# Kernel optimization log

Hardware: AMD Instinct MI355X
Metric: run time of the kernel (lower is better)

The kernel has to match this reference:

```python
import jax, jax.numpy as jnp
import numpy as np

N, D, T = 4096, 256, 32
GAMMA = 1.0 / 256.0  # 1/d
ALPHA = 1.0


def _rbf_kernel(X, Y, gamma):
    # K[i, j] = exp(-gamma * ||X[i] - Y[j]||^2), vectorized (replaces the
    # original per-(i,j) Python double loop).
    x2 = jnp.sum(X * X, axis=1)  # [n]
    y2 = jnp.sum(Y * Y, axis=1)  # [m]
    d2 = x2[:, None] + y2[None, :] - 2.0 * (X @ Y.T)  # [n, m]
    d2 = jnp.maximum(d2, 0.0)  # numerical guard; exact form is non-negative
    return jnp.exp(-gamma * d2)


def setup_inputs() -> dict:
    key = jax.random.key(0)
    kx, ky = jax.random.split(key)
    X = jax.random.normal(kx, (N, D), dtype=jnp.float32)
    y = jax.random.normal(ky, (N, T), dtype=jnp.float32)
    return {"X": X, "y": y}


def reference(X, y):
    # fit: K = rbf(X, X); dual = solve(K + alpha*I, y)
    K = _rbf_kernel(X, X, GAMMA)  # [N, N]
    A = K + ALPHA * jnp.eye(N, dtype=K.dtype)
    dual_coef = jnp.linalg.solve(A, y)  # [N, T]
    # predict(X): original recomputes rbf(X, X) == K, then K @ dual_coef
    y_pred = K @ dual_coef  # [N, T]
    return y_pred
```

## Files before the change

### kernel.cpp

```cpp
#include <hip/hip_runtime.h>
#include <math.h>

#define NN 4096
#define DD 256
#define TT 32
#define GAMMA (1.0f/256.0f)
#define ITERS 10
#define JBP 8
#define JCH 512
#define IB  128
#define BROW (JCH + 8)
#define KB_PAD 40

typedef __attribute__((ext_vector_type(8))) _Float16 f16x8;
typedef __attribute__((ext_vector_type(4))) _Float16 f16x4;
typedef __attribute__((ext_vector_type(4))) float f32x4;

__global__ __launch_bounds__(256) void setup(const float* __restrict__ X,
                                             float* __restrict__ x2,
                                             _Float16* __restrict__ Xh,
                                             const float* __restrict__ y,
                                             float* __restrict__ r, float* __restrict__ x,
                                             _Float16* __restrict__ vh,
                                             _Float16* __restrict__ vl,
                                             float* __restrict__ rrp) {
    const int b = blockIdx.x, tid = threadIdx.x;
    const int wid = tid >> 6, lane = tid & 63;
    if (b < 1024) {
        int row = b * 4 + wid;
        const float* xr = X + (size_t)row * DD;
        float4 v = *(const float4*)(xr + lane * 4);
        float s = v.x * v.x + v.y * v.y + v.z * v.z + v.w * v.w;
        #pragma unroll
        for (int o = 32; o; o >>= 1) s += __shfl_down(s, o);
        if (lane == 0) x2[row] = s;
        f16x4 h;
        h[0] = (_Float16)v.x; h[1] = (_Float16)v.y; h[2] = (_Float16)v.z; h[3] = (_Float16)v.w;
        *(f16x4*)(Xh + (size_t)row * DD + lane * 4) = h;
    } else {
        int bb = b - 1024;
        int t = bb >> 3, c = bb & 7;
        float s = 0.f;
        #pragma unroll
        for (int pass = 0; pass < 2; ++pass) {
            int i = c * 512 + pass * 256 + tid;
            float v = y[(size_t)i * TT + t];
            size_t off = (size_t)t * NN + i;
            r[off] = v; x[off] = 0.f;
            _Float16 h = (_Float16)v;
            vh[off] = h; vl[off] = (_Float16)(v - (float)h);
            s += v * v;
        }
        #pragma unroll
        for (int o = 32; o; o >>= 1) s += __shfl_down(s, o);
        __shared__ float red[4];
        if (lane == 0) red[wid] = s;
        __syncthreads();
        if (tid == 0) rrp[t * 8 + c] = red[0] + red[1] + red[2] + red[3];
    }
}

__global__ __launch_bounds__(256) void k_build(const _Float16* __restrict__ Xh,
                                               const float* __restrict__ x2,
                                               _Float16* __restrict__ Kh) {
    __shared__ _Float16 As[128 * KB_PAD];
    __shared__ _Float16 Bs[256 * KB_PAD];
    const int i0 = blockIdx.x * 128, j0 = blockIdx.y * 256;
    const int tid = threadIdx.x;
    const int wid = tid >> 6, lane = tid & 63;
    const int wr = wid >> 1, wc = wid & 1;
    const int l15 = lane & 15, l4 = lane >> 4;
    f32x4 acc[4][8] = {};
    for (int kc = 0; kc < DD; kc += 32) {
        __syncthreads();
        #pragma unroll
        for (int s = 0; s < 2; ++s) {
            int idx = s * 256 + tid;
            int row = idx >> 2, c = idx & 3;
            *(uint4*)(As + row * KB_PAD + c * 8) =
                *(const uint4*)(Xh + (size_t)(i0 + row) * DD + kc + c * 8);
        }
        #pragma unroll
        for (int s = 0; s < 4; ++s) {
            int idx = s * 256 + tid;
            int row = idx >> 2, c = idx & 3;
            *(uint4*)(Bs + row * KB_PAD + c * 8) =
                *(const uint4*)(Xh + (size_t)(j0 + row) * DD + kc + c * 8);
        }
        __syncthreads();
        f16x8 af[4], bfr[8];
        #pragma unroll
        for (int m = 0; m < 4; ++m)
            af[m] = *(const f16x8*)(As + (wr * 64 + m * 16 + l15) * KB_PAD + l4 * 8);
        #pragma unroll
        for (int n = 0; n < 8; ++n)
            bfr[n] = *(const f16x8*)(Bs + (wc * 128 + n * 16 + l15) * KB_PAD + l4 * 8);
        #pragma unroll
        for (int m = 0; m < 4; ++m)
            #pragma unroll
            for (int n = 0; n < 8; ++n)
                acc[m][n] = __builtin_amdgcn_mfma_f32_16x16x32_f16(af[m], bfr[n], acc[m][n], 0, 0, 0);
    }
    #pragma unroll
    for (int m = 0; m < 4; ++m) {
        #pragma unroll
        for (int rg = 0; rg < 4; ++rg) {
            int i = i0 + wr * 64 + m * 16 + l4 * 4 + rg;
            float x2i = x2[i];
            #pragma unroll
            for (int n = 0; n < 8; ++n) {
                int j = j0 + wc * 128 + n * 16 + l15;
                float d2 = fmaxf(x2i + x2[j] - 2.f * acc[m][n][rg], 0.f);
                Kh[(size_t)i * NN + j] = (_Float16)__expf(-GAMMA * d2);
            }
        }
    }
}

template<int RED>
__global__ __launch_bounds__(512) void matvec_part(const _Float16* __restrict__ Kh,
                                                   const _Float16* __restrict__ vh,
                                                   const _Float16* __restrict__ vl,
                                                   const float* __restrict__ r,
                                                   float* __restrict__ part,
                                                   float* __restrict__ rKvp) {
    __shared__ __align__(16) _Float16 Bbuf[2 * 32 * BROW];
    __shared__ float redb[8][33];
    _Float16* Bh = Bbuf;
    _Float16* Bl = Bbuf + 32 * BROW;
    const int ib = blockIdx.x;
    const int jb = blockIdx.y;
    const int bid = jb * 32 + ib;
    const int tid = threadIdx.x;
    const int wid = tid >> 6, lane = tid & 63;
    const int l15 = lane & 15, l4 = lane >> 4;
    #pragma unroll
    for (int s = 0; s < 4; ++s) {
        int c = s * 512 + tid;
        int row = c >> 6, col8 = c & 63;
        *(uint4*)(Bh + row * BROW + col8 * 8) =
            *(const uint4*)(vh + (size_t)row * NN + jb * JCH + col8 * 8);
        *(uint4*)(Bl + row * BROW + col8 * 8) =
            *(const uint4*)(vl + (size_t)row * NN + jb * JCH + col8 * 8);
    }
    __syncthreads();
    const _Float16* Ap  = Kh + (size_t)(ib * IB + wid * 16 + l15) * NN + jb * JCH + l4 * 8;
    const _Float16* bhp = Bh + l15 * BROW + l4 * 8;
    const _Float16* blp = Bl + l15 * BROW + l4 * 8;
    f32x4 acc0 = {}, acc1 = {};
    #pragma unroll 4
    for (int jc = 0; jc < JCH; jc += 32) {
        f16x8 a   = *(const f16x8*)(Ap + jc);
        f16x8 bh0 = *(const f16x8*)(bhp + jc);
        f16x8 bh1 = *(const f16x8*)(bhp + 16 * BROW + jc);
        f16x8 bl0 = *(const f16x8*)(blp + jc);
        f16x8 bl1 = *(const f16x8*)(blp + 16 * BROW + jc);
        acc0 = __builtin_amdgcn_mfma_f32_16x16x32_f16(a, bh0, acc0, 0, 0, 0);
        acc1 = __builtin_amdgcn_mfma_f32_16x16x32_f16(a, bh1, acc1, 0, 0, 0);
        acc0 = __builtin_amdgcn_mfma_f32_16x16x32_f16(a, bl0, acc0, 0, 0, 0);
        acc1 = __builtin_amdgcn_mfma_f32_16x16x32_f16(a, bl1, acc1, 0, 0, 0);
    }
    __syncthreads();
    float* tl = (float*)Bbuf;
    #pragma unroll
    for (int rg = 0; rg < 4; ++rg) {
        tl[(wid * 32 + l15) * 17 + l4 * 4 + rg]      = acc0[rg];
        tl[(wid * 32 + 16 + l15) * 17 + l4 * 4 + rg] = acc1[rg];
    }
    __syncthreads();
    #pragma unroll
    for (int q = 0; q < 8; ++q) {
        int idx = q * 64 + lane;
        int t = idx >> 4, il = idx & 15;
        int gi = ib * IB + wid * 16 + il;
        float val = tl[(wid * 32 + t) * 17 + il];
        part[((size_t)jb * TT + t) * NN + gi] = val;
        if (RED) {
            float cq = r[(size_t)t * NN + gi] * val;
            #pragma unroll
            for (int o = 8; o; o >>= 1) cq += __shfl_down(cq, o);
            if (il == 0) redb[wid][t] = cq;
        }
    }
    if (RED) {
        __syncthreads();
        if (tid < 32) {
            float s = 0.f;
            #pragma unroll
            for (int u = 0; u < 8; ++u) s += redb[u][tid];
            rKvp[tid * 256 + bid] = s;
        }
    }
}

__global__ __launch_bounds__(512) void cupd(const float* __restrict__ part, float* __restrict__ r,
                                            float* __restrict__ p, float* __restrict__ s_,
                                            float* __restrict__ x,
                                            _Float16* __restrict__ vh,
                                            _Float16* __restrict__ vl,
                                            const float* __restrict__ rrp_in,
                                            float* __restrict__ rrp_out,
                                            const float* __restrict__ rKvp,
                                            const float* __restrict__ scal_in,
                                            float* __restrict__ scal_out,
                                            int first, int last) {
    const int t = blockIdx.x, c = blockIdx.y, tid = threadIdx.x;
    const int wid = tid >> 6, lane = tid & 63;
    __shared__ float sc2[2];
    __shared__ float red[8];
    if (wid == 0) {
        float rw_ = 0.f;
        #pragma unroll
        for (int u = 0; u < 4; ++u) rw_ += rKvp[t * 256 + u * 64 + lane];
        float rr_ = (lane < 8) ? rrp_in[t * 8 + lane] : 0.f;
        #pragma unroll
        for (int o = 32; o; o >>= 1) { rw_ += __shfl_down(rw_, o); rr_ += __shfl_down(rr_, o); }
        if (lane == 0) {
            float rr = rr_;
            float rw = rw_ + rr;
            float alpha, beta;
            if (first) { beta = 0.f; alpha = rr / rw; }
            else {
                float ap = scal_in[t], rrprev = scal_in[TT + t];
                beta = rr / rrprev;
                alpha = rr / (rw - (beta / ap) * rr);
            }
            sc2[0] = alpha; sc2[1] = beta;
            if (c == 0) { scal_out[t] = alpha; scal_out[TT + t] = rr; }
        }
    }
    __syncthreads();
    const float alpha = sc2[0], beta = sc2[1];
    int i = c * 512 + tid;
    size_t off = (size_t)t * NN + i;
    float s = 0.f;
    #pragma unroll
    for (int b = 0; b < JBP; ++b) s += part[((size_t)b * TT + t) * NN + i];
    float rv = r[off];
    float wv = s + rv;
    float pn = first ? rv : fmaf(beta, p[off], rv);
    float sn = first ? wv : fmaf(beta, s_[off], wv);
    p[off] = pn; s_[off] = sn;
    float xn = x[off] + alpha * pn;
    x[off] = xn;
    float rn = rv - alpha * sn;
    r[off] = rn;
    float vout = last ? xn : rn;
    _Float16 h = (_Float16)vout;
    vh[off] = h; vl[off] = (_Float16)(vout - (float)h);
    float v = rn * rn;
    #pragma unroll
    for (int o = 32; o; o >>= 1) v += __shfl_down(v, o);
    if (lane == 0) red[wid] = v;
    __syncthreads();
    if (tid == 0) {
        float tot = 0.f;
        #pragma unroll
        for (int u = 0; u < 8; ++u) tot += red[u];
        rrp_out[t * 8 + c] = tot;
    }
}

__global__ __launch_bounds__(256) void predict_out(const float* __restrict__ part,
                                                   float* __restrict__ out) {
    __shared__ float st[TT][65];
    const int i0 = blockIdx.x * 64;
    const int tid = threadIdx.x;
    #pragma unroll
    for (int ph = 0; ph < 8; ++ph) {
        int idx = ph * 256 + tid;
        int il = idx & 63, t = idx >> 6;
        float s = 0.f;
        #pragma unroll
        for (int b = 0; b < JBP; ++b) s += part[((size_t)b * TT + t) * NN + i0 + il];
        st[t][il] = s;
    }
    __syncthreads();
    #pragma unroll
    for (int ph = 0; ph < 8; ++ph) {
        int idx = ph * 256 + tid;
        int t = idx & 31, il = idx >> 5;
        out[(size_t)(i0 + il) * TT + t] = st[t][il];
    }
}

extern "C" void kernel_launch(void* const* d_in, const int* in_sizes, int n_in,
                              void* d_out, int out_size, void* d_ws, size_t ws_size,
                              hipStream_t stream) {
    const float* X = (const float*)d_in[0];
    const float* y = (const float*)d_in[1];
    float* out = (float*)d_out;

    unsigned char* wsb = (unsigned char*)d_ws;
    _Float16* Kh = (_Float16*)wsb;  wsb += (size_t)NN * NN * 2;
    float* part  = (float*)wsb;     wsb += (size_t)JBP * TT * NN * 4;
    float* r     = (float*)wsb;     wsb += (size_t)TT * NN * 4;
    float* p     = (float*)wsb;     wsb += (size_t)TT * NN * 4;
    float* s_    = (float*)wsb;     wsb += (size_t)TT * NN * 4;
    float* x     = (float*)wsb;     wsb += (size_t)TT * NN * 4;
    _Float16* vh = (_Float16*)wsb;  wsb += (size_t)TT * NN * 2;
    _Float16* vl = (_Float16*)wsb;  wsb += (size_t)TT * NN * 2;
    _Float16* Xh = (_Float16*)wsb;  wsb += (size_t)NN * DD * 2;
    float* x2v   = (float*)wsb;     wsb += (size_t)NN * 4;
    float* rrp   = (float*)wsb;     wsb += 512 * 4;
    float* rKvp  = (float*)wsb;     wsb += (size_t)TT * 256 * 4;
    float* scal  = (float*)wsb;     wsb += 128 * 4;

    setup<<<1280, 256, 0, stream>>>(X, x2v, Xh, y, r, x, vh, vl, rrp);
    k_build<<<dim3(NN / 128, NN / 256), 256, 0, stream>>>(Xh, x2v, Kh);

    for (int j = 0; j < ITERS; ++j) {
        matvec_part<1><<<dim3(32, JBP), 512, 0, stream>>>(Kh, vh, vl, r, part, rKvp);
        cupd<<<dim3(TT, 8), 512, 0, stream>>>(part, r, p, s_, x, vh, vl,
                                              rrp + (j & 1) * 256, rrp + ((j + 1) & 1) * 256,
                                              rKvp,
                                              scal + (j & 1) * 64, scal + ((j + 1) & 1) * 64,
                                              j == 0 ? 1 : 0, j == ITERS - 1 ? 1 : 0);
    }

    matvec_part<0><<<dim3(32, JBP), 512, 0, stream>>>(Kh, vh, vl, nullptr, part, nullptr);
    predict_out<<<NN / 64, 256, 0, stream>>>(part, out);
}
```

Before: 204.3 us.

## Track K·x via CG recurrence to drop final matvec; widen k_build K-chunk

Result: faster. 191.8 us (-6.1%).

```diff
diff --git a/kernel.cpp b/kernel.cpp
--- a/kernel.cpp
+++ b/kernel.cpp
@@ -10,7 +10,8 @@
 #define JCH 512
 #define IB  128
 #define BROW (JCH + 8)
-#define KB_PAD 40
+#define KC  64
+#define KBP 72
 
 typedef __attribute__((ext_vector_type(8))) _Float16 f16x8;
 typedef __attribute__((ext_vector_type(4))) _Float16 f16x4;
@@ -20,7 +21,7 @@
                                              float* __restrict__ x2,
                                              _Float16* __restrict__ Xh,
                                              const float* __restrict__ y,
-                                             float* __restrict__ r, float* __restrict__ x,
+                                             float* __restrict__ r,
                                              _Float16* __restrict__ vh,
                                              _Float16* __restrict__ vl,
                                              float* __restrict__ rrp) {
@@ -46,7 +47,7 @@
             int i = c * 512 + pass * 256 + tid;
             float v = y[(size_t)i * TT + t];
             size_t off = (size_t)t * NN + i;
-            r[off] = v; x[off] = 0.f;
+            r[off] = v;
             _Float16 h = (_Float16)v;
             vh[off] = h; vl[off] = (_Float16)(v - (float)h);
             s += v * v;
@@ -63,43 +64,46 @@
 __global__ __launch_bounds__(256) void k_build(const _Float16* __restrict__ Xh,
                                                const float* __restrict__ x2,
                                                _Float16* __restrict__ Kh) {
-    __shared__ _Float16 As[128 * KB_PAD];
-    __shared__ _Float16 Bs[256 * KB_PAD];
+    __shared__ _Float16 As[128 * KBP];
+    __shared__ _Float16 Bs[256 * KBP];
     const int i0 = blockIdx.x * 128, j0 = blockIdx.y * 256;
     const int tid = threadIdx.x;
     const int wid = tid >> 6, lane = tid & 63;
     const int wr = wid >> 1, wc = wid & 1;
     const int l15 = lane & 15, l4 = lane >> 4;
     f32x4 acc[4][8] = {};
-    for (int kc = 0; kc < DD; kc += 32) {
+    for (int kc = 0; kc < DD; kc += KC) {
         __syncthreads();
-        #pragma unroll
-        for (int s = 0; s < 2; ++s) {
-            int idx = s * 256 + tid;
-            int row = idx >> 2, c = idx & 3;
-            *(uint4*)(As + row * KB_PAD + c * 8) =
-                *(const uint4*)(Xh + (size_t)(i0 + row) * DD + kc + c * 8);
-        }
         #pragma unroll
         for (int s = 0; s < 4; ++s) {
             int idx = s * 256 + tid;
-            int row = idx >> 2, c = idx & 3;
-            *(uint4*)(Bs + row * KB_PAD + c * 8) =
+            int row = idx >> 3, c = idx & 7;
+            *(uint4*)(As + row * KBP + c * 8) =
+                *(const uint4*)(Xh + (size_t)(i0 + row) * DD + kc + c * 8);
+        }
+        #pragma unroll
+        for (int s = 0; s < 8; ++s) {
+            int idx = s * 256 + tid;
+            int row = idx >> 3, c = idx & 7;
+            *(uint4*)(Bs + row * KBP + c * 8) =
                 *(const uint4*)(Xh + (size_t)(j0 + row) * DD + kc + c * 8);
         }
         __syncthreads();
-        f16x8 af[4], bfr[8];
-        #pragma unroll
-        for (int m = 0; m < 4; ++m)
-            af[m] = *(const f16x8*)(As + (wr * 64 + m * 16 + l15) * KB_PAD + l4 * 8);
-        #pragma unroll
-        for (int n = 0; n < 8; ++n)
-            bfr[n] = *(const f16x8*)(Bs + (wc * 128 + n * 16 + l15) * KB_PAD + l4 * 8);
-        #pragma unroll
-        for (int m = 0; m < 4; ++m)
+        #pragma unroll
+        for (int kk = 0; kk < 2; ++kk) {
+            f16x8 af[4], bfr[8];
+            #pragma unroll
+            for (int m = 0; m < 4; ++m)
+                af[m] = *(const f16x8*)(As + (wr * 64 + m * 16 + l15) * KBP + kk * 32 + l4 * 8);
             #pragma unroll
             for (int n = 0; n < 8; ++n)
-                acc[m][n] = __builtin_amdgcn_mfma_f32_16x16x32_f16(af[m], bfr[n], acc[m][n], 0, 0, 0);
+                bfr[n] = *(const f16x8*)(Bs + (wc * 128 + n * 16 + l15) * KBP + kk * 32 + l4 * 8);
+            #pragma unroll
+            for (int m = 0; m < 4; ++m)
+                #pragma unroll
+                for (int n = 0; n < 8; ++n)
+                    acc[m][n] = __builtin_amdgcn_mfma_f32_16x16x32_f16(af[m], bfr[n], acc[m][n], 0, 0, 0);
+        }
     }
     #pragma unroll
     for (int m = 0; m < 4; ++m) {
@@ -117,7 +121,6 @@
     }
 }
 
-template<int RED>
 __global__ __launch_bounds__(512) void matvec_part(const _Float16* __restrict__ Kh,
                                                    const _Float16* __restrict__ vh,
                                                    const _Float16* __restrict__ vl,
@@ -175,27 +178,23 @@
         int gi = ib * IB + wid * 16 + il;
         float val = tl[(wid * 32 + t) * 17 + il];
         part[((size_t)jb * TT + t) * NN + gi] = val;
-        if (RED) {
-            float cq = r[(size_t)t * NN + gi] * val;
-            #pragma unroll
-            for (int o = 8; o; o >>= 1) cq += __shfl_down(cq, o);
-            if (il == 0) redb[wid][t] = cq;
-        }
-    }
-    if (RED) {
-        __syncthreads();
-        if (tid < 32) {
-            float s = 0.f;
-            #pragma unroll
-            for (int u = 0; u < 8; ++u) s += redb[u][tid];
-            rKvp[tid * 256 + bid] = s;
-        }
+        float cq = r[(size_t)t * NN + gi] * val;
+        #pragma unroll
+        for (int o = 8; o; o >>= 1) cq += __shfl_down(cq, o);
+        if (il == 0) redb[wid][t] = cq;
+    }
+    __syncthreads();
+    if (tid < 32) {
+        float s = 0.f;
+        #pragma unroll
+        for (int u = 0; u < 8; ++u) s += redb[u][tid];
+        rKvp[tid * 256 + bid] = s;
     }
 }
 
 __global__ __launch_bounds__(512) void cupd(const float* __restrict__ part, float* __restrict__ r,
                                             float* __restrict__ p, float* __restrict__ s_,
-                                            float* __restrict__ x,
+                                            float* __restrict__ x, float* __restrict__ ax,
                                             _Float16* __restrict__ vh,
                                             _Float16* __restrict__ vl,
                                             const float* __restrict__ rrp_in,
@@ -203,6 +202,7 @@
                                             const float* __restrict__ rKvp,
                                             const float* __restrict__ scal_in,
                                             float* __restrict__ scal_out,
+                                            float* __restrict__ out,
                                             int first, int last) {
     const int t = blockIdx.x, c = blockIdx.y, tid = threadIdx.x;
     const int wid = tid >> 6, lane = tid & 63;
@@ -241,13 +241,17 @@
     float pn = first ? rv : fmaf(beta, p[off], rv);
     float sn = first ? wv : fmaf(beta, s_[off], wv);
     p[off] = pn; s_[off] = sn;
-    float xn = x[off] + alpha * pn;
-    x[off] = xn;
+    float xn  = (first ? 0.f : x[off])  + alpha * pn;
+    float axn = (first ? 0.f : ax[off]) + alpha * sn;
+    x[off] = xn; ax[off] = axn;
     float rn = rv - alpha * sn;
     r[off] = rn;
-    float vout = last ? xn : rn;
-    _Float16 h = (_Float16)vout;
-    vh[off] = h; vl[off] = (_Float16)(vout - (float)h);
+    if (last) {
+        out[(size_t)i * TT + t] = axn - xn;
+    } else {
+        _Float16 h = (_Float16)rn;
+        vh[off] = h; vl[off] = (_Float16)(rn - (float)h);
+    }
     float v = rn * rn;
     #pragma unroll
     for (int o = 32; o; o >>= 1) v += __shfl_down(v, o);
@@ -258,29 +262,6 @@
         #pragma unroll
         for (int u = 0; u < 8; ++u) tot += red[u];
         rrp_out[t * 8 + c] = tot;
-    }
-}
-
-__global__ __launch_bounds__(256) void predict_out(const float* __restrict__ part,
-                                                   float* __restrict__ out) {
-    __shared__ float st[TT][65];
-    const int i0 = blockIdx.x * 64;
-    const int tid = threadIdx.x;
-    #pragma unroll
-    for (int ph = 0; ph < 8; ++ph) {
-        int idx = ph * 256 + tid;
-        int il = idx & 63, t = idx >> 6;
-        float s = 0.f;
-        #pragma unroll
-        for (int b = 0; b < JBP; ++b) s += part[((size_t)b * TT + t) * NN + i0 + il];
-        st[t][il] = s;
-    }
-    __syncthreads();
-    #pragma unroll
-    for (int ph = 0; ph < 8; ++ph) {
-        int idx = ph * 256 + tid;
-        int t = idx & 31, il = idx >> 5;
-        out[(size_t)(i0 + il) * TT + t] = st[t][il];
     }
 }
 
@@ -298,6 +279,7 @@
     float* p     = (float*)wsb;     wsb += (size_t)TT * NN * 4;
     float* s_    = (float*)wsb;     wsb += (size_t)TT * NN * 4;
     float* x     = (float*)wsb;     wsb += (size_t)TT * NN * 4;
+    float* ax    = (float*)wsb;     wsb += (size_t)TT * NN * 4;
     _Float16* vh = (_Float16*)wsb;  wsb += (size_t)TT * NN * 2;
     _Float16* vl = (_Float16*)wsb;  wsb += (size_t)TT * NN * 2;
     _Float16* Xh = (_Float16*)wsb;  wsb += (size_t)NN * DD * 2;
@@ -306,18 +288,16 @@
     float* rKvp  = (float*)wsb;     wsb += (size_t)TT * 256 * 4;
     float* scal  = (float*)wsb;     wsb += 128 * 4;
 
-    setup<<<1280, 256, 0, stream>>>(X, x2v, Xh, y, r, x, vh, vl, rrp);
+    setup<<<1280, 256, 0, stream>>>(X, x2v, Xh, y, r, vh, vl, rrp);
     k_build<<<dim3(NN / 128, NN / 256), 256, 0, stream>>>(Xh, x2v, Kh);
 
     for (int j = 0; j < ITERS; ++j) {
-        matvec_part<1><<<dim3(32, JBP), 512, 0, stream>>>(Kh, vh, vl, r, part, rKvp);
-        cupd<<<dim3(TT, 8), 512, 0, stream>>>(part, r, p, s_, x, vh, vl,
+        matvec_part<<<dim3(32, JBP), 512, 0, stream>>>(Kh, vh, vl, r, part, rKvp);
+        cupd<<<dim3(TT, 8), 512, 0, stream>>>(part, r, p, s_, x, ax, vh, vl,
                                               rrp + (j & 1) * 256, rrp + ((j + 1) & 1) * 256,
                                               rKvp,
                                               scal + (j & 1) * 64, scal + ((j + 1) & 1) * 64,
+                                              out,
                                               j == 0 ? 1 : 0, j == ITERS - 1 ? 1 : 0);
     }
-
-    matvec_part<0><<<dim3(32, JBP), 512, 0, stream>>>(Kh, vh, vl, nullptr, part, nullptr);
-    predict_out<<<NN / 64, 256, 0, stream>>>(part, out);
-}
+}
```
